# Optimization experiments

Measured on AMD Instinct MI355X. Metric: run time of the kernel, lower is better.

The kernel has to match this reference:

```python
import jax, jax.numpy as jnp
import numpy as np

HEADS = 16
DIM_HEAD = 64


def setup_inputs() -> dict:
    key = jax.random.key(0)
    k1, k2, k3, k4 = jax.random.split(key, 4)
    b, sq, skv, dim = 2, 2048, 2048, 1024
    inner = HEADS * DIM_HEAD
    return {
        "x_q": jax.random.normal(k1, (b, sq, dim), dtype=jnp.float32),
        "x_kv": jax.random.normal(k2, (b, skv, dim), dtype=jnp.float32),
        "W_qkv": jax.random.normal(k3, (dim, 3 * inner), dtype=jnp.float32) * (dim ** -0.5),
        "W_out": jax.random.normal(k4, (inner, dim), dtype=jnp.float32) * (inner ** -0.5),
        "b_out": jnp.zeros((dim,), dtype=jnp.float32),
    }


def reference(x_q, x_kv, W_qkv, W_out, b_out):
    b, sq, dim = x_q.shape
    skv = x_kv.shape[1]
    inner = HEADS * DIM_HEAD
    scale = DIM_HEAD ** -0.5
    # to_qkv on concat([x_q, x_kv], seq) as in the original (bias-free linear)
    qkv = jnp.concatenate([x_q, x_kv], axis=1) @ W_qkv  # [b, sq+skv, 3*inner]
    q, k, v = jnp.split(qkv, 3, axis=-1)
    q = q[:, :sq].reshape(b, sq, HEADS, DIM_HEAD).transpose(0, 2, 1, 3)   # [b,h,sq,d]
    k = k[:, sq:].reshape(b, skv, HEADS, DIM_HEAD).transpose(0, 2, 1, 3)  # [b,h,skv,d]
    v = v[:, sq:].reshape(b, skv, HEADS, DIM_HEAD).transpose(0, 2, 1, 3)  # [b,h,skv,d]
    dots = jnp.einsum('bhqd,bhkd->bhqk', q, k) * scale
    attn = jax.nn.softmax(dots, axis=-1)  # dropout p=0.0 -> identity
    out = jnp.einsum('bhqk,bhkd->bhqd', attn, v)
    out = out.transpose(0, 2, 1, 3).reshape(b, sq, inner)
    return out @ W_out + b_out
```

## Files before the change

### kernel.cpp

```cpp
#include <hip/hip_runtime.h>


typedef __attribute__((ext_vector_type(8))) short short8;
typedef __attribute__((ext_vector_type(4))) short short4v;
typedef __attribute__((ext_vector_type(4))) float floatx4;
typedef __attribute__((ext_vector_type(16))) float floatx16;

#define QSCALE 0.18033688f

#if __has_builtin(__builtin_amdgcn_exp2f)
#define EXP2(x) __builtin_amdgcn_exp2f(x)
#else
#define EXP2(x) exp2f(x)
#endif

__device__ __forceinline__ ushort f2b(float f) {
  union { float f; unsigned u; } x; x.f = f;
  unsigned r = (x.u + 0x7fffu + ((x.u >> 16) & 1u)) >> 16;
  return (ushort)r;
}

__device__ __forceinline__ unsigned f2b2(float a, float b) {
  union { float f; unsigned u; } x, y; x.f = a; y.f = b;
  return __builtin_amdgcn_perm(y.u + 0x8000u, x.u + 0x8000u, 0x07060302u);
}

__device__ __forceinline__ unsigned cvtpk(float a, float b) {
  unsigned r;
  asm("v_cvt_pk_bf16_f32 %0, %1, %2" : "=v"(r) : "v"(a), "v"(b));
  return r;
}

#define GLL(gp, lp)                                                            \
  __builtin_amdgcn_global_load_lds(                                            \
      (const __attribute__((address_space(1))) void*)(gp),                     \
      (__attribute__((address_space(3))) void*)(lp), 16, 0, 0)

__global__ void prep(const float* __restrict__ xq, const float* __restrict__ xkv,
                     ushort* __restrict__ oq, ushort* __restrict__ okv,
                     const float* __restrict__ Wqkv, ushort* __restrict__ WqkvT,
                     const float* __restrict__ Wout, ushort* __restrict__ WoutT) {
  __shared__ float tile[32][33];
  int bid = blockIdx.x;
  const int n = 4096 * 1024;
  if (bid < 2048) {
    bool lo = bid < 1024;
    const float* in = lo ? xq : xkv;
    ushort* out = lo ? oq : okv;
    int b2 = lo ? bid : bid - 1024;
    int stride = 1024 * 256 * 4;
    for (int i = (b2 * 256 + (int)threadIdx.x) * 4; i < n; i += stride) {
      float4 v = *(const float4*)(in + i);
      uint2 o;
      o.x = f2b2(v.x, v.y);
      o.y = f2b2(v.z, v.w);
      *(uint2*)(out + i) = o;
    }
    return;
  }
  int tb = bid - 2048;
  int bx = tb & 127, by = tb >> 7;
  bool first = bx < 96;
  const float* in = first ? Wqkv : Wout;
  ushort* out = first ? WqkvT : WoutT;
  int N = first ? 3072 : 1024;
  int bxx = first ? bx : bx - 96;
  int k0 = by * 32, n0 = bxx * 32;
  int tx = threadIdx.x & 31, ty = threadIdx.x >> 5;
#pragma unroll
  for (int i = 0; i < 32; i += 8)
    tile[ty + i][tx] = in[(size_t)(k0 + ty + i) * N + n0 + tx];
  __syncthreads();
#pragma unroll
  for (int i = 0; i < 32; i += 8)
    out[(size_t)(n0 + ty + i) * 1024 + k0 + tx] = f2b(tile[tx][ty + i]);
}

__global__ __launch_bounds__(256, 3) void gemm_qkv(
    const ushort* __restrict__ Aq, const ushort* __restrict__ Akv,
    const ushort* __restrict__ Bt,
    ushort* __restrict__ Cq, ushort* __restrict__ Ck, ushort* __restrict__ Cv) {
  __shared__ __align__(16) ushort smem[17408];
  ushort* Asb = smem;
  ushort* Bsb = smem + 8192;
  const int n0 = blockIdx.x * 128, m0 = blockIdx.y * 128;
  const ushort* A = (blockIdx.x >= 8) ? Akv : Aq;
  const int t = threadIdx.x;
  const int w = t >> 6, lane = t & 63, dl = lane & 15, g = lane >> 4;
  const int wm = (w >> 1) * 64, wn = (w & 1) * 64;
  const int K = 1024;

  auto stage = [&](int buf, int k0) {
#pragma unroll
    for (int p = 0; p < 2; p++) {
      int j = t + p * 256;
      int row = j >> 2, slot = j & 3, c = (slot - row) & 3;
      GLL(A + (size_t)(m0 + row) * K + k0 + c * 8, &Asb[buf * 4096 + j * 8]);
    }
#pragma unroll
    for (int p = 0; p < 2; p++) {
      int j = t + p * 256;
      int row = j >> 2, slot = j & 3, c = (slot - row) & 3;
      GLL(Bt + (size_t)(n0 + row) * K + k0 + c * 8, &Bsb[buf * 4096 + j * 8]);
    }
  };

  const floatx4 fz = {0.f, 0.f, 0.f, 0.f};
  floatx4 acc[4][4];
#pragma unroll
  for (int i = 0; i < 4; i++)
#pragma unroll
    for (int j = 0; j < 4; j++) acc[i][j] = fz;

  stage(0, 0);
  for (int kt = 0; kt < 32; kt++) {
    int cur = kt & 1;
    __builtin_amdgcn_s_waitcnt(0);
    __syncthreads();
    if (kt + 1 < 32) stage(cur ^ 1, (kt + 1) * 32);
    short8 af[4], bf[4];
#pragma unroll
    for (int mt = 0; mt < 4; mt++) {
      int row = wm + mt * 16 + dl;
      af[mt] = *(const short8*)&Asb[cur * 4096 + row * 32 + ((g + row) & 3) * 8];
    }
#pragma unroll
    for (int nt = 0; nt < 4; nt++) {
      int row = wn + nt * 16 + dl;
      bf[nt] = *(const short8*)&Bsb[cur * 4096 + row * 32 + ((g + row) & 3) * 8];
    }
#pragma unroll
    for (int mt = 0; mt < 4; mt++)
#pragma unroll
      for (int nt = 0; nt < 4; nt++)
        acc[mt][nt] = __builtin_amdgcn_mfma_f32_16x16x32_bf16(af[mt], bf[nt], acc[mt][nt], 0, 0, 0);
  }

  if (blockIdx.x < 16) {
#pragma unroll
    for (int mt = 0; mt < 4; mt++)
#pragma unroll
      for (int nt = 0; nt < 4; nt++) {
        int gcol = n0 + wn + nt * 16 + dl;
        int row0 = m0 + wm + mt * 16 + g * 4;
        if (gcol < 1024) {
#pragma unroll
          for (int r = 0; r < 4; r++)
            Cq[(size_t)(row0 + r) * 1024 + gcol] = f2b(acc[mt][nt][r] * QSCALE);
        } else {
#pragma unroll
          for (int r = 0; r < 4; r++)
            Ck[(size_t)(row0 + r) * 1024 + gcol - 1024] = f2b(acc[mt][nt][r]);
        }
      }
  } else {
    __syncthreads();
#pragma unroll
    for (int mt = 0; mt < 4; mt++)
#pragma unroll
      for (int nt = 0; nt < 4; nt++) {
        int ncol = wn + nt * 16 + dl;
        int mrow = wm + mt * 16 + g * 4;
        uint2 pk;
        pk.x = f2b2(acc[mt][nt][0], acc[mt][nt][1]);
        pk.y = f2b2(acc[mt][nt][2], acc[mt][nt][3]);
        *(uint2*)&smem[ncol * 136 + mrow] = pk;
      }
    __syncthreads();
    int hd0 = n0 - 2048;
    int bb = m0 >> 11;
    int kv0 = m0 & 2047;
#pragma unroll
    for (int p = 0; p < 8; p++) {
      int j = t + p * 256;
      int row = j >> 4, c = j & 15;
      short8 v = *(const short8*)&smem[row * 136 + c * 8];
      *(short8*)(Cv + ((size_t)(bb * 1024 + hd0 + row)) * 2048 + kv0 + c * 8) = v;
    }
  }
}

__global__ __launch_bounds__(256, 3) void gemm_out(
    const ushort* __restrict__ A, const ushort* __restrict__ Bt,
    float* __restrict__ C, const float* __restrict__ bias) {
  __shared__ __align__(16) ushort As[2][128 * 64];
  __shared__ __align__(16) ushort Bs[2][64 * 64];
  const int n0 = blockIdx.x * 64, m0 = blockIdx.y * 128;
  const int t = threadIdx.x;
  const int w = t >> 6, lane = t & 63, dl = lane & 15, g = lane >> 4;
  const int wm = (w >> 1) * 64, wn = (w & 1) * 32;
  const int K = 1024;

  auto stage = [&](int buf, int k0) {
#pragma unroll
    for (int p = 0; p < 4; p++) {
      int j = t + p * 256;
      int row = j >> 3, slot = j & 7, c = (slot - row) & 7;
      GLL(A + (size_t)(m0 + row) * K + k0 + c * 8, &As[buf][j * 8]);
    }
#pragma unroll
    for (int p = 0; p < 2; p++) {
      int j = t + p * 256;
      int row = j >> 3, slot = j & 7, c = (slot - row) & 7;
      GLL(Bt + (size_t)(n0 + row) * K + k0 + c * 8, &Bs[buf][j * 8]);
    }
  };

  const floatx4 fz = {0.f, 0.f, 0.f, 0.f};
  floatx4 acc[4][2];
#pragma unroll
  for (int i = 0; i < 4; i++)
#pragma unroll
    for (int j = 0; j < 2; j++) acc[i][j] = fz;

  stage(0, 0);
  for (int kt = 0; kt < 16; kt++) {
    int cur = kt & 1;
    __builtin_amdgcn_s_waitcnt(0);
    __syncthreads();
    if (kt + 1 < 16) stage(cur ^ 1, (kt + 1) * 64);
#pragma unroll
    for (int ks = 0; ks < 2; ks++) {
      short8 af[4], bf[2];
#pragma unroll
      for (int mt = 0; mt < 4; mt++) {
        int row = wm + mt * 16 + dl;
        af[mt] = *(const short8*)&As[cur][row * 64 + ((ks * 4 + g + row) & 7) * 8];
      }
#pragma unroll
      for (int nt = 0; nt < 2; nt++) {
        int row = wn + nt * 16 + dl;
        bf[nt] = *(const short8*)&Bs[cur][row * 64 + ((ks * 4 + g + row) & 7) * 8];
      }
#pragma unroll
      for (int mt = 0; mt < 4; mt++)
#pragma unroll
        for (int nt = 0; nt < 2; nt++)
          acc[mt][nt] = __builtin_amdgcn_mfma_f32_16x16x32_bf16(af[mt], bf[nt], acc[mt][nt], 0, 0, 0);
    }
  }
#pragma unroll
  for (int mt = 0; mt < 4; mt++)
#pragma unroll
    for (int nt = 0; nt < 2; nt++) {
      int gcol = n0 + wn + nt * 16 + dl;
      int row0 = m0 + wm + mt * 16 + g * 4;
      float badd = bias[gcol];
#pragma unroll
      for (int r = 0; r < 4; r++)
        C[(size_t)(row0 + r) * 1024 + gcol] = acc[mt][nt][r] + badd;
    }
}

__global__ __launch_bounds__(512, 4) void attn(
    const ushort* __restrict__ Qb,
    const ushort* __restrict__ Kb,
    const ushort* __restrict__ Vt,
    ushort* __restrict__ Ob) {
  __shared__ __align__(16) ushort Ks[2][2][64 * 64];
  __shared__ __align__(16) ushort Vs[2][2][64 * 64];

  const int bh = blockIdx.x, b = bh >> 4, h = bh & 15;
  const int q0 = blockIdx.y * 128;
  const int t = threadIdx.x, w = t >> 6, lane = t & 63;
  const int l31 = lane & 31, l5 = lane >> 5;
  const int qw = w & 3, kvh = w >> 2;
  const int th = t & 255;

  const ushort* Kg = Kb + (size_t)(b * 2048 + kvh * 1024) * 1024 + h * 64;
  const ushort* Vg = Vt + (size_t)(b * 1024 + h * 64) * 2048 + kvh * 1024;

  short8 bq[4];
  {
    int qa = q0 + qw * 32 + l31;
    const ushort* qrow = Qb + (size_t)(b * 2048 + qa) * 1024 + h * 64;
#pragma unroll
    for (int ks = 0; ks < 4; ks++)
      bq[ks] = *(const short8*)(qrow + ks * 16 + l5 * 8);
  }

  auto stageK = [&](int buf, int kv0) {
#pragma unroll
    for (int p = 0; p < 2; p++) {
      int j = th + p * 256;
      int row = j >> 3, slot = j & 7, c = (slot - row) & 7;
      GLL(Kg + (size_t)(kv0 + row) * 1024 + c * 8, &Ks[kvh][buf][j * 8]);
    }
  };
  auto stageV = [&](int buf, int kv0) {
#pragma unroll
    for (int p = 0; p < 2; p++) {
      int j = th + p * 256;
      int row = j >> 3, slot = j & 7, c = (slot - row) & 7;
      GLL(Vg + (size_t)row * 2048 + kv0 + c * 8, &Vs[kvh][buf][j * 8]);
    }
  };
  stageK(0, 0);
  stageV(0, 0);

  floatx16 o2[2];
#pragma unroll
  for (int m2 = 0; m2 < 2; m2++)
#pragma unroll
    for (int r = 0; r < 16; r++) o2[m2][r] = 0.f;
  floatx4 l4 = {0.f, 0.f, 0.f, 0.f};

  for (int it = 0; it < 16; it++) {
    int cur = it & 1;
    __builtin_amdgcn_s_waitcnt(0);
    __syncthreads();
    if (it + 1 < 16) { stageK(cur ^ 1, (it + 1) * 64); stageV(cur ^ 1, (it + 1) * 64); }

    short8 bp[4];
#pragma unroll
    for (int m2 = 0; m2 < 2; m2++) {
      floatx16 s;
#pragma unroll
      for (int r = 0; r < 16; r++) s[r] = 0.f;
      int row = m2 * 32 + l31;
      __builtin_amdgcn_s_setprio(1);
#pragma unroll
      for (int ks = 0; ks < 4; ks++) {
        short8 a = *(const short8*)
            &Ks[kvh][cur][row * 64 + ((ks * 2 + l5 + row) & 7) * 8];
        s = __builtin_amdgcn_mfma_f32_32x32x16_bf16(a, bq[ks], s, 0, 0, 0);
      }
      __builtin_amdgcn_s_setprio(0);
#pragma unroll
      for (int r = 0; r < 16; r++) s[r] = EXP2(s[r]);
#pragma unroll
      for (int r = 0; r < 16; r++) l4[r & 3] += s[r];
      unsigned pk[8];
#pragma unroll
      for (int p = 0; p < 8; p++)
        pk[p] = cvtpk(s[2 * p], s[2 * p + 1]);
#pragma unroll
      for (int hf = 0; hf < 2; hf++) {
        unsigned x0 = pk[hf * 4 + 0], y0 = pk[hf * 4 + 2];
        unsigned x1 = pk[hf * 4 + 1], y1 = pk[hf * 4 + 3];
        asm("v_permlane32_swap_b32 %0, %1" : "+v"(x0), "+v"(y0));
        asm("v_permlane32_swap_b32 %0, %1" : "+v"(x1), "+v"(y1));
        union { unsigned u[4]; short8 s8; } fu;
        fu.u[0] = x0; fu.u[1] = x1; fu.u[2] = y0; fu.u[3] = y1;
        bp[m2 * 2 + hf] = fu.s8;
      }
    }

    __builtin_amdgcn_s_setprio(1);
#pragma unroll
    for (int kt = 0; kt < 4; kt++)
#pragma unroll
      for (int m2 = 0; m2 < 2; m2++) {
        int row = m2 * 32 + l31;
        short8 av = *(const short8*)
            &Vs[kvh][cur][row * 64 + ((kt * 2 + l5 + row) & 7) * 8];
        o2[m2] = __builtin_amdgcn_mfma_f32_32x32x16_bf16(av, bp[kt], o2[m2], 0, 0, 0);
      }
    __builtin_amdgcn_s_setprio(0);
  }

  float lp = (l4[0] + l4[1]) + (l4[2] + l4[3]);

  __syncthreads();
  float2* Of = (float2*)&Ks[0][0][0];
  float*  Lf = (float*)&Vs[0][0][0];
  if (kvh == 1) {
#pragma unroll
    for (int m2 = 0; m2 < 2; m2++)
#pragma unroll
      for (int p = 0; p < 8; p++) {
        float2 v = {o2[m2][2 * p], o2[m2][2 * p + 1]};
        Of[(m2 * 8 + p) * 256 + qw * 64 + lane] = v;
      }
    Lf[qw * 64 + lane] = lp;
  }
  __syncthreads();
  if (kvh == 0) {
#pragma unroll
    for (int m2 = 0; m2 < 2; m2++)
#pragma unroll
      for (int p = 0; p < 8; p++) {
        float2 v = Of[(m2 * 8 + p) * 256 + qw * 64 + lane];
        o2[m2][2 * p] += v.x;
        o2[m2][2 * p + 1] += v.y;
      }
    lp += Lf[qw * 64 + lane];
  }
  float l = lp + __shfl_xor(lp, 32);
  float inv_l = 1.f / l;

  __syncthreads();
  ushort* Ot = &Ks[0][0][0];
  if (kvh == 0) {
    int q = qw * 32 + l31;
#pragma unroll
    for (int m2 = 0; m2 < 2; m2++)
#pragma unroll
      for (int pp = 0; pp < 4; pp++) {
        uint2 pk2;
        pk2.x = cvtpk(o2[m2][4 * pp + 0] * inv_l, o2[m2][4 * pp + 1] * inv_l);
        pk2.y = cvtpk(o2[m2][4 * pp + 2] * inv_l, o2[m2][4 * pp + 3] * inv_l);
        int s = m2 * 8 + 2 * pp + l5;
        *(uint2*)&Ot[q * 64 + ((s + q) & 15) * 4] = pk2;
      }
  }
  asm volatile("" ::: "memory");
  if (kvh == 0) {
#pragma unroll
    for (int p = 0; p < 4; p++) {
      int j = lane + p * 64;
      int r32 = j >> 3, c = j & 7;
      int qr = qw * 32 + r32;
      short4v lo = *(const short4v*)&Ot[qr * 64 + ((2 * c + qr) & 15) * 4];
      short4v hi = *(const short4v*)&Ot[qr * 64 + ((2 * c + 1 + qr) & 15) * 4];
      short8 v = {lo.x, lo.y, lo.z, lo.w, hi.x, hi.y, hi.z, hi.w};
      *(short8*)(Ob + (size_t)(b * 2048 + q0 + qr) * 1024 + h * 64 + c * 8) = v;
    }
  }
}

extern "C" void kernel_launch(void* const* d_in, const int* in_sizes, int n_in,
                              void* d_out, int out_size, void* d_ws, size_t ws_size,
                              hipStream_t stream) {
  const float* x_q  = (const float*)d_in[0];
  const float* x_kv = (const float*)d_in[1];
  const float* Wqkv = (const float*)d_in[2];
  const float* Wout = (const float*)d_in[3];
  const float* bout = (const float*)d_in[4];
  float* out = (float*)d_out;

  char* p = (char*)d_ws;
  ushort* Xq    = (ushort*)p; p += (size_t)4096 * 1024 * 2;
  ushort* Xkv   = (ushort*)p; p += (size_t)4096 * 1024 * 2;
  ushort* WqkvT = (ushort*)p; p += (size_t)3072 * 1024 * 2;
  ushort* WoutT = (ushort*)p; p += (size_t)1024 * 1024 * 2;
  ushort* Qb    = (ushort*)p; p += (size_t)4096 * 1024 * 2;
  ushort* Kb    = (ushort*)p; p += (size_t)4096 * 1024 * 2;
  ushort* Vt    = (ushort*)p; p += (size_t)2 * 1024 * 2048 * 2;
  ushort* Ob    = (ushort*)p; p += (size_t)4096 * 1024 * 2;

  prep<<<6144, 256, 0, stream>>>(x_q, x_kv, Xq, Xkv, Wqkv, WqkvT, Wout, WoutT);
  gemm_qkv<<<dim3(24, 32), 256, 0, stream>>>(Xq, Xkv, WqkvT, Qb, Kb, Vt);
  attn<<<dim3(32, 16), 512, 0, stream>>>(Qb, Kb, Vt, Ob);
  gemm_out<<<dim3(16, 32), 256, 0, stream>>>(Ob, WoutT, out, bout);
}
```

Measured before the change: 192.1 us.

## Halve attention block threads and give each wave two query tiles

The attention kernel now runs with 256 threads instead of 512. Each wave handles two 32-row query tiles, so every K and V fragment read from LDS feeds two MFMAs instead of one. This cuts LDS read traffic per MFMA and the number of waves sharing each staged tile. In exchange it roughly doubles accumulator registers per wave (four floatx16 O tiles plus S tiles), which can lower occupancy or cause spills, and each thread now issues twice as many staging loads. The output write-back is rewritten so all threads store after an added barrier.

```diff
diff --git a/kernel.cpp b/kernel.cpp
--- a/kernel.cpp
+++ b/kernel.cpp
@@ -252,7 +252,7 @@
     }
 }
 
-__global__ __launch_bounds__(512, 4) void attn(
+__global__ __launch_bounds__(256, 2) void attn(
     const ushort* __restrict__ Qb,
     const ushort* __restrict__ Kb,
     const ushort* __restrict__ Vt,
@@ -264,33 +264,34 @@
   const int q0 = blockIdx.y * 128;
   const int t = threadIdx.x, w = t >> 6, lane = t & 63;
   const int l31 = lane & 31, l5 = lane >> 5;
-  const int qw = w & 3, kvh = w >> 2;
-  const int th = t & 255;
+  const int qw = w & 1, kvh = w >> 1;
+  const int th = t & 127;
 
   const ushort* Kg = Kb + (size_t)(b * 2048 + kvh * 1024) * 1024 + h * 64;
   const ushort* Vg = Vt + (size_t)(b * 1024 + h * 64) * 2048 + kvh * 1024;
 
-  short8 bq[4];
-  {
-    int qa = q0 + qw * 32 + l31;
+  short8 bq[2][4];
+#pragma unroll
+  for (int qt = 0; qt < 2; qt++) {
+    int qa = q0 + qw * 64 + qt * 32 + l31;
     const ushort* qrow = Qb + (size_t)(b * 2048 + qa) * 1024 + h * 64;
 #pragma unroll
     for (int ks = 0; ks < 4; ks++)
-      bq[ks] = *(const short8*)(qrow + ks * 16 + l5 * 8);
+      bq[qt][ks] = *(const short8*)(qrow + ks * 16 + l5 * 8);
   }
 
   auto stageK = [&](int buf, int kv0) {
 #pragma unroll
-    for (int p = 0; p < 2; p++) {
-      int j = th + p * 256;
+    for (int p = 0; p < 4; p++) {
+      int j = th + p * 128;
       int row = j >> 3, slot = j & 7, c = (slot - row) & 7;
       GLL(Kg + (size_t)(kv0 + row) * 1024 + c * 8, &Ks[kvh][buf][j * 8]);
     }
   };
   auto stageV = [&](int buf, int kv0) {
 #pragma unroll
-    for (int p = 0; p < 2; p++) {
-      int j = th + p * 256;
+    for (int p = 0; p < 4; p++) {
+      int j = th + p * 128;
       int row = j >> 3, slot = j & 7, c = (slot - row) & 7;
       GLL(Vg + (size_t)row * 2048 + kv0 + c * 8, &Vs[kvh][buf][j * 8]);
     }
@@ -298,12 +299,14 @@
   stageK(0, 0);
   stageV(0, 0);
 
-  floatx16 o2[2];
-#pragma unroll
-  for (int m2 = 0; m2 < 2; m2++)
-#pragma unroll
-    for (int r = 0; r < 16; r++) o2[m2][r] = 0.f;
-  floatx4 l4 = {0.f, 0.f, 0.f, 0.f};
+  floatx16 o2[2][2];
+#pragma unroll
+  for (int qt = 0; qt < 2; qt++)
+#pragma unroll
+    for (int m2 = 0; m2 < 2; m2++)
+#pragma unroll
+      for (int r = 0; r < 16; r++) o2[qt][m2][r] = 0.f;
+  floatx4 l4q[2] = {{0.f, 0.f, 0.f, 0.f}, {0.f, 0.f, 0.f, 0.f}};
 
   for (int it = 0; it < 16; it++) {
     int cur = it & 1;
@@ -311,38 +314,43 @@
     __syncthreads();
     if (it + 1 < 16) { stageK(cur ^ 1, (it + 1) * 64); stageV(cur ^ 1, (it + 1) * 64); }
 
-    short8 bp[4];
+    short8 bp[2][4];
 #pragma unroll
     for (int m2 = 0; m2 < 2; m2++) {
-      floatx16 s;
-#pragma unroll
-      for (int r = 0; r < 16; r++) s[r] = 0.f;
+      floatx16 s0, s1;
+#pragma unroll
+      for (int r = 0; r < 16; r++) { s0[r] = 0.f; s1[r] = 0.f; }
       int row = m2 * 32 + l31;
       __builtin_amdgcn_s_setprio(1);
 #pragma unroll
       for (int ks = 0; ks < 4; ks++) {
         short8 a = *(const short8*)
             &Ks[kvh][cur][row * 64 + ((ks * 2 + l5 + row) & 7) * 8];
-        s = __builtin_amdgcn_mfma_f32_32x32x16_bf16(a, bq[ks], s, 0, 0, 0);
+        s0 = __builtin_amdgcn_mfma_f32_32x32x16_bf16(a, bq[0][ks], s0, 0, 0, 0);
+        s1 = __builtin_amdgcn_mfma_f32_32x32x16_bf16(a, bq[1][ks], s1, 0, 0, 0);
       }
       __builtin_amdgcn_s_setprio(0);
 #pragma unroll
-      for (int r = 0; r < 16; r++) s[r] = EXP2(s[r]);
-#pragma unroll
-      for (int r = 0; r < 16; r++) l4[r & 3] += s[r];
-      unsigned pk[8];
-#pragma unroll
-      for (int p = 0; p < 8; p++)
-        pk[p] = cvtpk(s[2 * p], s[2 * p + 1]);
-#pragma unroll
-      for (int hf = 0; hf < 2; hf++) {
-        unsigned x0 = pk[hf * 4 + 0], y0 = pk[hf * 4 + 2];
-        unsigned x1 = pk[hf * 4 + 1], y1 = pk[hf * 4 + 3];
-        asm("v_permlane32_swap_b32 %0, %1" : "+v"(x0), "+v"(y0));
-        asm("v_permlane32_swap_b32 %0, %1" : "+v"(x1), "+v"(y1));
-        union { unsigned u[4]; short8 s8; } fu;
-        fu.u[0] = x0; fu.u[1] = x1; fu.u[2] = y0; fu.u[3] = y1;
-        bp[m2 * 2 + hf] = fu.s8;
+      for (int qt = 0; qt < 2; qt++) {
+        floatx16& s = qt ? s1 : s0;
+#pragma unroll
+        for (int r = 0; r < 16; r++) s[r] = EXP2(s[r]);
+#pragma unroll
+        for (int r = 0; r < 16; r++) l4q[qt][r & 3] += s[r];
+        unsigned pk[8];
+#pragma unroll
+        for (int p = 0; p < 8; p++)
+          pk[p] = cvtpk(s[2 * p], s[2 * p + 1]);
+#pragma unroll
+        for (int hf = 0; hf < 2; hf++) {
+          unsigned x0 = pk[hf * 4 + 0], y0 = pk[hf * 4 + 2];
+          unsigned x1 = pk[hf * 4 + 1], y1 = pk[hf * 4 + 3];
+          asm("v_permlane32_swap_b32 %0, %1" : "+v"(x0), "+v"(y0));
+          asm("v_permlane32_swap_b32 %0, %1" : "+v"(x1), "+v"(y1));
+          union { unsigned u[4]; short8 s8; } fu;
+          fu.u[0] = x0; fu.u[1] = x1; fu.u[2] = y0; fu.u[3] = y1;
+          bp[qt][m2 * 2 + hf] = fu.s8;
+        }
       }
     }
 
@@ -354,68 +362,84 @@
         int row = m2 * 32 + l31;
         short8 av = *(const short8*)
             &Vs[kvh][cur][row * 64 + ((kt * 2 + l5 + row) & 7) * 8];
-        o2[m2] = __builtin_amdgcn_mfma_f32_32x32x16_bf16(av, bp[kt], o2[m2], 0, 0, 0);
+        o2[0][m2] = __builtin_amdgcn_mfma_f32_32x32x16_bf16(av, bp[0][kt], o2[0][m2], 0, 0, 0);
+        o2[1][m2] = __builtin_amdgcn_mfma_f32_32x32x16_bf16(av, bp[1][kt], o2[1][m2], 0, 0, 0);
       }
     __builtin_amdgcn_s_setprio(0);
   }
 
-  float lp = (l4[0] + l4[1]) + (l4[2] + l4[3]);
+  float lp[2];
+#pragma unroll
+  for (int qt = 0; qt < 2; qt++)
+    lp[qt] = (l4q[qt][0] + l4q[qt][1]) + (l4q[qt][2] + l4q[qt][3]);
 
   __syncthreads();
   float2* Of = (float2*)&Ks[0][0][0];
   float*  Lf = (float*)&Vs[0][0][0];
   if (kvh == 1) {
 #pragma unroll
-    for (int m2 = 0; m2 < 2; m2++)
-#pragma unroll
-      for (int p = 0; p < 8; p++) {
-        float2 v = {o2[m2][2 * p], o2[m2][2 * p + 1]};
-        Of[(m2 * 8 + p) * 256 + qw * 64 + lane] = v;
-      }
-    Lf[qw * 64 + lane] = lp;
+    for (int qt = 0; qt < 2; qt++) {
+#pragma unroll
+      for (int m2 = 0; m2 < 2; m2++)
+#pragma unroll
+        for (int p = 0; p < 8; p++) {
+          float2 v = {o2[qt][m2][2 * p], o2[qt][m2][2 * p + 1]};
+          Of[(((qw * 2 + qt) * 2 + m2) * 8 + p) * 64 + lane] = v;
+        }
+      Lf[(qw * 2 + qt) * 64 + lane] = lp[qt];
+    }
   }
   __syncthreads();
   if (kvh == 0) {
 #pragma unroll
-    for (int m2 = 0; m2 < 2; m2++)
-#pragma unroll
-      for (int p = 0; p < 8; p++) {
-        float2 v = Of[(m2 * 8 + p) * 256 + qw * 64 + lane];
-        o2[m2][2 * p] += v.x;
-        o2[m2][2 * p + 1] += v.y;
-      }
-    lp += Lf[qw * 64 + lane];
-  }
-  float l = lp + __shfl_xor(lp, 32);
-  float inv_l = 1.f / l;
+    for (int qt = 0; qt < 2; qt++) {
+#pragma unroll
+      for (int m2 = 0; m2 < 2; m2++)
+#pragma unroll
+        for (int p = 0; p < 8; p++) {
+          float2 v = Of[(((qw * 2 + qt) * 2 + m2) * 8 + p) * 64 + lane];
+          o2[qt][m2][2 * p] += v.x;
+          o2[qt][m2][2 * p + 1] += v.y;
+        }
+      lp[qt] += Lf[(qw * 2 + qt) * 64 + lane];
+    }
+  }
+  float inv_l[2];
+#pragma unroll
+  for (int qt = 0; qt < 2; qt++) {
+    float l = lp[qt] + __shfl_xor(lp[qt], 32);
+    inv_l[qt] = 1.f / l;
+  }
 
   __syncthreads();
   ushort* Ot = &Ks[0][0][0];
   if (kvh == 0) {
-    int q = qw * 32 + l31;
-#pragma unroll
-    for (int m2 = 0; m2 < 2; m2++)
-#pragma unroll
-      for (int pp = 0; pp < 4; pp++) {
-        uint2 pk2;
-        pk2.x = cvtpk(o2[m2][4 * pp + 0] * inv_l, o2[m2][4 * pp + 1] * inv_l);
-        pk2.y = cvtpk(o2[m2][4 * pp + 2] * inv_l, o2[m2][4 * pp + 3] * inv_l);
-        int s = m2 * 8 + 2 * pp + l5;
-        *(uint2*)&Ot[q * 64 + ((s + q) & 15) * 4] = pk2;
-      }
-  }
-  asm volatile("" ::: "memory");
-  if (kvh == 0) {
-#pragma unroll
-    for (int p = 0; p < 4; p++) {
-      int j = lane + p * 64;
-      int r32 = j >> 3, c = j & 7;
-      int qr = qw * 32 + r32;
-      short4v lo = *(const short4v*)&Ot[qr * 64 + ((2 * c + qr) & 15) * 4];
-      short4v hi = *(const short4v*)&Ot[qr * 64 + ((2 * c + 1 + qr) & 15) * 4];
-      short8 v = {lo.x, lo.y, lo.z, lo.w, hi.x, hi.y, hi.z, hi.w};
-      *(short8*)(Ob + (size_t)(b * 2048 + q0 + qr) * 1024 + h * 64 + c * 8) = v;
-    }
+#pragma unroll
+    for (int qt = 0; qt < 2; qt++) {
+      int q = qw * 64 + qt * 32 + l31;
+#pragma unroll
+      for (int m2 = 0; m2 < 2; m2++)
+#pragma unroll
+        for (int pp = 0; pp < 4; pp++) {
+          uint2 pk2;
+          pk2.x = cvtpk(o2[qt][m2][4 * pp + 0] * inv_l[qt],
+                        o2[qt][m2][4 * pp + 1] * inv_l[qt]);
+          pk2.y = cvtpk(o2[qt][m2][4 * pp + 2] * inv_l[qt],
+                        o2[qt][m2][4 * pp + 3] * inv_l[qt]);
+          int s = m2 * 8 + 2 * pp + l5;
+          *(uint2*)&Ot[q * 64 + ((s + q) & 15) * 4] = pk2;
+        }
+    }
+  }
+  __syncthreads();
+#pragma unroll
+  for (int p = 0; p < 4; p++) {
+    int j = t + p * 256;
+    int qr = j >> 3, c = j & 7;
+    short4v lo = *(const short4v*)&Ot[qr * 64 + ((2 * c + qr) & 15) * 4];
+    short4v hi = *(const short4v*)&Ot[qr * 64 + ((2 * c + 1 + qr) & 15) * 4];
+    short8 v = {lo.x, lo.y, lo.z, lo.w, hi.x, hi.y, hi.z, hi.w};
+    *(short8*)(Ob + (size_t)(b * 2048 + q0 + qr) * 1024 + h * 64 + c * 8) = v;
   }
 }
 
@@ -441,6 +465,6 @@
 
   prep<<<6144, 256, 0, stream>>>(x_q, x_kv, Xq, Xkv, Wqkv, WqkvT, Wout, WoutT);
   gemm_qkv<<<dim3(24, 32), 256, 0, stream>>>(Xq, Xkv, WqkvT, Qb, Kb, Vt);
-  attn<<<dim3(32, 16), 512, 0, stream>>>(Qb, Kb, Vt, Ob);
+  attn<<<dim3(32, 16), 256, 0, stream>>>(Qb, Kb, Vt, Ob);
   gemm_out<<<dim3(16, 32), 256, 0, stream>>>(Ob, WoutT, out, bout);
 }
```

Result: no change. 191.1 us (-0.5%).
